# Kernel optimization log

Hardware: AMD Instinct MI355X
Metric: run time of the kernel (lower is better)

Reference implementation:

```python
import jax, jax.numpy as jnp
import numpy as np
from jax import lax

MAX_DEG = 10
BATCH = 4096
PER_DEG = 50000              # atoms per degree bucket
N_ATOMS = PER_DEG * (MAX_DEG + 1)
F = 128                      # n_atom_features == nb_filter
EPS = 1e-5


def setup_inputs() -> dict:
    key = jax.random.key(0)
    ks = jax.random.split(key, 8)
    atoms = jax.random.normal(ks[0], (N_ATOMS, F), jnp.float32)
    # atoms sorted by degree: degree d occupies rows [d*PER_DEG, (d+1)*PER_DEG)
    deg_slice = jnp.stack([jnp.arange(MAX_DEG + 1) * PER_DEG,
                           jnp.full((MAX_DEG + 1,), PER_DEG)], axis=1).astype(jnp.int32)
    membership = jax.random.randint(ks[1], (N_ATOMS,), 0, BATCH, dtype=jnp.int32)
    inp = {"atoms": atoms, "deg_slice": deg_slice, "membership": membership}
    for d in range(1, MAX_DEG + 1):
        inp[f"adj_{d}"] = jax.random.randint(jax.random.fold_in(key, d),
                                             (PER_DEG, d), 0, N_ATOMS, dtype=jnp.int32)
    inp["W"] = jax.random.normal(ks[2], (2 * MAX_DEG + 1, F, F), jnp.float32) * 0.05
    inp["b"] = jnp.zeros((2 * MAX_DEG + 1, F), jnp.float32)
    inp["gW"] = jax.random.normal(ks[3], (MAX_DEG + 1, F, F), jnp.float32) * 0.05
    inp["gb"] = jnp.zeros((MAX_DEG + 1, F), jnp.float32)
    inp["gamma"] = jnp.ones((F,), jnp.float32)
    inp["beta"] = jnp.zeros((F,), jnp.float32)
    return inp


def reference(atoms, deg_slice, membership,
              adj_1, adj_2, adj_3, adj_4, adj_5, adj_6, adj_7, adj_8, adj_9, adj_10,
              W, b, gW, gb, gamma, beta):
    adjs = [adj_1, adj_2, adj_3, adj_4, adj_5, adj_6, adj_7, adj_8, adj_9, adj_10]
    rel_outs = [None] * (MAX_DEG + 1)
    gat_outs = [None] * (MAX_DEG + 1)
    for d in range(1, MAX_DEG + 1):
        nbr_sum = jnp.take(atoms, adjs[d - 1], axis=0).sum(axis=1)  # (PER_DEG, F)
        self_atoms = lax.dynamic_slice_in_dim(atoms, deg_slice[d, 0], PER_DEG, axis=0)
        rel_outs[d] = (nbr_sum @ W[2 * (d - 1)] + b[2 * (d - 1)]
                       + self_atoms @ W[2 * (d - 1) + 1] + b[2 * (d - 1) + 1])
        gat_outs[d] = self_atoms @ gW[d - 1] + gb[d - 1]
    # degree 0 (min_deg == 0): self transform only
    self0 = lax.dynamic_slice_in_dim(atoms, deg_slice[0, 0], PER_DEG, axis=0)
    rel_outs[0] = self0 @ W[2 * MAX_DEG] + b[2 * MAX_DEG]
    gat_outs[0] = self0 @ gW[MAX_DEG] + gb[MAX_DEG]

    activated = jnp.concatenate(rel_outs, axis=0)     # (N_ATOMS, F), degree order == atom order
    gather_atoms = jnp.concatenate(gat_outs, axis=0)  # (N_ATOMS, F)
    # graph_gather: per-molecule sum (tf.dynamic_partition + reduce_sum == segment_sum)
    graph_feat = jax.ops.segment_sum(gather_atoms, membership, num_segments=BATCH)
    # activation is 'linear' (identity); layer-norm on atom features as in call()
    m = activated.mean(axis=-1, keepdims=True)
    std = jnp.sqrt(activated.var(axis=-1, keepdims=True) + EPS)
    normed = gamma * ((activated - m) / (std + EPS)) + beta
    return normed, graph_feat
```

## Files before the change

### kernel.cpp

```cpp
#include <hip/hip_runtime.h>
#include <hip/hip_bf16.h>

#define F_DIM   128
#define PER_DEG 50000
#define NDEG    11
#define MAXD    10
#define BATCH   4096
#define N_ATOMS (PER_DEG * NDEG)

#define BM     64
#define LDSN   136
#define BPD    ((PER_DEG + BM - 1) / BM)
#define WT_K   256
#define GWT_K  1440
#define LDST_L 264
#define WT_K_L 384

typedef __attribute__((ext_vector_type(4))) float f32x4;
typedef __attribute__((ext_vector_type(8))) short short8v;
typedef __attribute__((ext_vector_type(4))) short short4v;

struct AdjPtrs { const int* p[MAXD]; };

__device__ inline short bf16bits(float x) {
    __hip_bfloat16 h = __float2bfloat16(x);
    return __builtin_bit_cast(short, h);
}
__device__ inline float bf_lo(unsigned u) { return __builtin_bit_cast(float, u << 16); }
__device__ inline float bf_hi(unsigned u) { return __builtin_bit_cast(float, u & 0xFFFF0000u); }
__device__ inline float bf2f(short s) {
    return __builtin_bit_cast(float, ((unsigned)(unsigned short)s) << 16);
}
__device__ inline unsigned enc4_i8(float x0, float x1, float x2, float x3) {
    int q0 = (int)rintf(x0 * 16.0f), q1 = (int)rintf(x1 * 16.0f);
    int q2 = (int)rintf(x2 * 16.0f), q3 = (int)rintf(x3 * 16.0f);
    q0 = max(-127, min(127, q0)); q1 = max(-127, min(127, q1));
    q2 = max(-127, min(127, q2)); q3 = max(-127, min(127, q3));
    return (unsigned)(q0 & 255) | ((unsigned)(q1 & 255) << 8) |
           ((unsigned)(q2 & 255) << 16) | ((unsigned)(q3 & 255) << 24);
}
__device__ inline int sbyte(unsigned w, int k) {
    return (int)(w << (24 - 8 * k)) >> 24;
}

__global__ void prep_wt_main(const float* __restrict__ W, short* __restrict__ wt) {
    int idx = blockIdx.x * blockDim.x + threadIdx.x;
    const int total = NDEG * F_DIM * WT_K;
    if (idx >= total) return;
    int d   = idx / (F_DIM * WT_K);
    int rem = idx % (F_DIM * WT_K);
    int c   = rem / WT_K;
    int k   = rem % WT_K;
    float v;
    if (d == 0) {
        v = (k < 128) ? 0.0f : W[20 * 16384 + (k - 128) * F_DIM + c];
    } else {
        int wi = (k < 128) ? (2 * (d - 1)) : (2 * (d - 1) + 1);
        v = W[wi * 16384 + (k & 127) * F_DIM + c];
    }
    wt[idx] = bf16bits(v);
}

__global__ void prep_gwt(const float* __restrict__ gW, const float* __restrict__ gb,
                         short* __restrict__ gwt) {
    int idx = blockIdx.x * blockDim.x + threadIdx.x;
    const int total = F_DIM * GWT_K;
    if (idx >= total) return;
    int c = idx / GWT_K;
    int k = idx % GWT_K;
    float v = 0.0f;
    if (k < 1408) {
        int dd = k >> 7, f = k & 127;
        int gi = dd ? (dd - 1) : 10;
        v = gW[gi * 16384 + f * F_DIM + c];
    } else if (k < 1419) {
        int dd = k - 1408;
        int gi = dd ? (dd - 1) : 10;
        v = gb[gi * F_DIM + c];
    }
    gwt[idx] = bf16bits(v);
}

__global__ void to_i8(const float* __restrict__ in, unsigned char* __restrict__ out8) {
    const size_t n8 = (size_t)N_ATOMS * F_DIM / 8;
    size_t stride = (size_t)gridDim.x * blockDim.x;
    for (size_t k = (size_t)blockIdx.x * blockDim.x + threadIdx.x; k < n8; k += stride) {
        f32x4 a = __builtin_nontemporal_load((const f32x4*)in + 2 * k);
        f32x4 c = __builtin_nontemporal_load((const f32x4*)in + 2 * k + 1);
        uint2 u;
        u.x = enc4_i8(a[0], a[1], a[2], a[3]);
        u.y = enc4_i8(c[0], c[1], c[2], c[3]);
        ((uint2*)out8)[k] = u;
    }
}

__global__ void hist_kernel(const int* __restrict__ mem, int* __restrict__ hist2) {
    int i = blockIdx.x * blockDim.x + threadIdx.x;
    if (i >= N_ATOMS) return;
    atomicAdd(&hist2[mem[i] * NDEG + i / PER_DEG], 1);
}

__global__ void scan_offsets(const int* __restrict__ hist2,
                             int* __restrict__ off, int* __restrict__ cur) {
    __shared__ int lds[1024];
    const int tid = threadIdx.x;
    int h[4][NDEG];
    int tsum = 0;
    #pragma unroll
    for (int mi = 0; mi < 4; ++mi) {
        int m = tid * 4 + mi;
        #pragma unroll
        for (int dd = 0; dd < NDEG; ++dd) { h[mi][dd] = hist2[m * NDEG + dd]; tsum += h[mi][dd]; }
    }
    lds[tid] = tsum;
    __syncthreads();
    for (int ofs = 1; ofs < 1024; ofs <<= 1) {
        int v = (tid >= ofs) ? lds[tid - ofs] : 0;
        __syncthreads();
        lds[tid] += v;
        __syncthreads();
    }
    int run = lds[tid] - tsum;
    #pragma unroll
    for (int mi = 0; mi < 4; ++mi) {
        int m = tid * 4 + mi;
        #pragma unroll
        for (int dd = 0; dd < NDEG; ++dd) {
            int k = m * NDEG + dd;
            off[k] = run; cur[k] = run;
            run += h[mi][dd];
        }
    }
}

__global__ void scatter_kernel(const int* __restrict__ mem,
                               int* __restrict__ cur, int* __restrict__ idx) {
    int i = blockIdx.x * blockDim.x + threadIdx.x;
    if (i >= N_ATOMS) return;
    int pos = atomicAdd(&cur[mem[i] * NDEG + i / PER_DEG], 1);
    idx[pos] = i;
}

__global__ __launch_bounds__(256, 4) void fused_deg(
    const unsigned char* __restrict__ ai8,
    AdjPtrs adj,
    const short* __restrict__ wt,
    const float* __restrict__ b,
    const float* __restrict__ gamma,
    const float* __restrict__ beta,
    float* __restrict__ outN)
{
    __shared__ short As[BM * LDSN];
    const int bid   = blockIdx.x;
    const int d     = bid % NDEG;
    const int rb    = bid / NDEG;
    const int rows0 = rb * BM;
    const int tid   = threadIdx.x;

    {
        const int rloc = tid >> 2;
        const int p    = tid & 3;
        const int grow = rows0 + rloc;
        short* basep = &As[rloc * LDSN + p * 32];
        int acci[32];
        #pragma unroll
        for (int e = 0; e < 32; ++e) acci[e] = 0;
        if (grow < PER_DEG && d > 0) {
            const int* ar = adj.p[d - 1] + (size_t)grow * d;
            int idxs[MAXD];
            #pragma unroll
            for (int j = 0; j < MAXD; ++j) idxs[j] = (j < d) ? ar[j] : 0;
            uint4 b0x, b0y, b1x, b1y, b2x, b2y;
            {
                const uint4* r0 = (const uint4*)(ai8 + (size_t)idxs[0] * F_DIM) + p * 2;
                b0x = r0[0]; b0y = r0[1];
            }
            if (d > 1) {
                const uint4* r1 = (const uint4*)(ai8 + (size_t)idxs[1] * F_DIM) + p * 2;
                b1x = r1[0]; b1y = r1[1];
            }
            #pragma unroll
            for (int j = 0; j < MAXD; ++j) {
                if (j < d) {
                    if (j + 2 < d) {
                        const uint4* rn =
                            (const uint4*)(ai8 + (size_t)idxs[j + 2] * F_DIM) + p * 2;
                        b2x = rn[0]; b2y = rn[1];
                    }
                    unsigned wds[8] = { b0x.x, b0x.y, b0x.z, b0x.w,
                                        b0y.x, b0y.y, b0y.z, b0y.w };
                    #pragma unroll
                    for (int dw = 0; dw < 8; ++dw) {
                        #pragma unroll
                        for (int k = 0; k < 4; ++k)
                            acci[dw * 4 + k] += sbyte(wds[dw], k);
                    }
                    b0x = b1x; b0y = b1y;
                    b1x = b2x; b1y = b2y;
                }
            }
        }
        #pragma unroll
        for (int q = 0; q < 4; ++q) {
            short8v nb;
            #pragma unroll
            for (int e = 0; e < 8; ++e)
                nb[e] = bf16bits((float)acci[q * 8 + e] * 0.0625f);
            *(short8v*)(basep + q * 8) = nb;
        }
    }
    __syncthreads();

    const int w  = tid >> 6;
    const int l  = tid & 63;
    const int cg = l & 15;
    const int rg = l >> 4;

    short8v a[8];
    const short* arow = &As[(w * 16 + cg) * LDSN + rg * 8];
    #pragma unroll
    for (int s = 0; s < 4; ++s) a[s] = *(const short8v*)(arow + s * 32);
    int srow = d * PER_DEG + rows0 + w * 16 + cg;
    if (srow >= N_ATOMS) srow = N_ATOMS - 1;
    {
        const unsigned char* sp8 = ai8 + (size_t)srow * F_DIM + rg * 8;
        #pragma unroll
        for (int s = 0; s < 4; ++s) {
            uint2 u = *(const uint2*)(sp8 + s * 32);
            short8v sv;
            #pragma unroll
            for (int e = 0; e < 8; ++e) {
                unsigned wd = (e < 4) ? u.x : u.y;
                sv[e] = bf16bits((float)sbyte(wd, e & 3) * 0.0625f);
            }
            a[4 + s] = sv;
        }
    }

    const short* wtd = wt + (size_t)d * F_DIM * WT_K;
    f32x4 aA[8];
    #pragma unroll
    for (int n = 0; n < 8; ++n) aA[n] = 0.0f;
    #pragma unroll
    for (int s = 0; s < 8; ++s) {
        #pragma unroll
        for (int n = 0; n < 8; ++n) {
            short8v bv = *(const short8v*)(wtd + (n * 16 + cg) * WT_K + s * 32 + rg * 8);
            aA[n] = __builtin_amdgcn_mfma_f32_16x16x32_bf16(a[s], bv, aA[n], 0, 0, 0);
        }
    }

    float biasv[8], gam[8], bet[8];
    #pragma unroll
    for (int n = 0; n < 8; ++n) {
        int col = n * 16 + cg;
        biasv[n] = (d > 0) ? (b[(2 * d - 2) * F_DIM + col] + b[(2 * d - 1) * F_DIM + col])
                           : b[20 * F_DIM + col];
        gam[n] = gamma[col];
        bet[n] = beta[col];
    }
    const int valid = (PER_DEG - rows0 < BM) ? (PER_DEG - rows0) : BM;
    #pragma unroll
    for (int j = 0; j < 4; ++j) {
        const int rl = w * 16 + rg * 4 + j;
        float x[8];
        float s1 = 0.f, s2 = 0.f;
        #pragma unroll
        for (int n = 0; n < 8; ++n) {
            x[n] = aA[n][j] + biasv[n];
            s1 += x[n];
            s2 += x[n] * x[n];
        }
        #pragma unroll
        for (int m = 1; m < 16; m <<= 1) {
            s1 += __shfl_xor(s1, m);
            s2 += __shfl_xor(s2, m);
        }
        float mean = s1 * (1.0f / 128.0f);
        float var  = fmaxf(s2 * (1.0f / 128.0f) - mean * mean, 0.0f);
        float inv  = 1.0f / (sqrtf(var + 1e-5f) + 1e-5f);
        if (rl < valid) {
            float* op = outN + (size_t)(d * PER_DEG + rows0 + rl) * F_DIM;
            #pragma unroll
            for (int n = 0; n < 8; ++n)
                op[n * 16 + cg] = gam[n] * ((x[n] - mean) * inv) + bet[n];
        }
    }
}

__global__ __launch_bounds__(128) void mol_reduce(
    const float* __restrict__ atoms, const int* __restrict__ idx,
    const int* __restrict__ off, const int* __restrict__ hist2,
    short* __restrict__ sums)
{
    const int key = blockIdx.x;
    const int m   = key / NDEG;
    const int dd  = key - m * NDEG;
    const int c   = threadIdx.x;
    const int base = off[key];
    const int n    = hist2[key];
    float acc = 0.0f;
    if (n > 0) {
        int id0 = idx[base];
        float vcur = atoms[(size_t)id0 * F_DIM + c];
        for (int t = 0; t < n; ++t) {
            float vnext = 0.0f;
            if (t + 1 < n) {
                int id1 = idx[base + t + 1];
                vnext = atoms[(size_t)id1 * F_DIM + c];
            }
            acc += vcur;
            vcur = vnext;
        }
    }
    short* out = sums + (size_t)m * GWT_K;
    out[dd * F_DIM + c] = bf16bits(acc);
    if (c == 0) out[1408 + dd] = bf16bits((float)n);
    if (dd == 0 && c >= 11 && c < 32) out[1408 + c] = 0;
}

__global__ __launch_bounds__(256) void gat_gemm(
    const short* __restrict__ sums, const short* __restrict__ gwt,
    float* __restrict__ outG)
{
    const int rows0 = blockIdx.x * 64;
    const int tid = threadIdx.x;
    const int w = tid >> 6, l = tid & 63, cg = l & 15, rg = l >> 4;
    const short* ap = sums + (size_t)(rows0 + w * 16 + cg) * GWT_K + rg * 8;
    f32x4 acc[8];
    #pragma unroll
    for (int n = 0; n < 8; ++n) acc[n] = 0.0f;
    for (int ks = 0; ks < GWT_K / 32; ++ks) {
        short8v av = *(const short8v*)(ap + ks * 32);
        #pragma unroll
        for (int n = 0; n < 8; ++n) {
            short8v bv = *(const short8v*)(gwt + (size_t)(n * 16 + cg) * GWT_K + ks * 32 + rg * 8);
            acc[n] = __builtin_amdgcn_mfma_f32_16x16x32_bf16(av, bv, acc[n], 0, 0, 0);
        }
    }
    #pragma unroll
    for (int j = 0; j < 4; ++j) {
        int r = rows0 + w * 16 + rg * 4 + j;
        #pragma unroll
        for (int n = 0; n < 8; ++n)
            outG[(size_t)r * F_DIM + n * 16 + cg] = acc[n][j];
    }
}

__global__ void prep_wt_full(const float* __restrict__ W, const float* __restrict__ gW,
                             short* __restrict__ wt) {
    int idx = blockIdx.x * blockDim.x + threadIdx.x;
    const int total = NDEG * F_DIM * WT_K_L;
    if (idx >= total) return;
    int d   = idx / (F_DIM * WT_K_L);
    int rem = idx % (F_DIM * WT_K_L);
    int c   = rem / WT_K_L;
    int k   = rem % WT_K_L;
    float v;
    if (k < 256) {
        if (d == 0) v = (k < 128) ? 0.0f : W[20 * 16384 + (k - 128) * F_DIM + c];
        else {
            int wi = (k < 128) ? (2 * (d - 1)) : (2 * (d - 1) + 1);
            v = W[wi * 16384 + (k & 127) * F_DIM + c];
        }
    } else {
        int gi = (d == 0) ? 10 : (d - 1);
        v = gW[gi * 16384 + (k - 256) * F_DIM + c];
    }
    wt[idx] = bf16bits(v);
}

__global__ __launch_bounds__(256, 2) void fused_legacy(
    const float* __restrict__ atoms,
    const int* __restrict__ membership, AdjPtrs adj,
    const short* __restrict__ wt, const float* __restrict__ b,
    const float* __restrict__ gb, const float* __restrict__ gamma,
    const float* __restrict__ beta, float* __restrict__ outN, float* __restrict__ outG)
{
    __shared__ short As[BM * LDST_L];
    const int bid = blockIdx.x, d = bid / BPD, rb = bid % BPD;
    const int rows0 = rb * BM, tid = threadIdx.x;
    {
        const int rloc = tid >> 2, p = tid & 3;
        const int grow = rows0 + rloc;
        const bool rv = grow < PER_DEG;
        short* basep = &As[rloc * LDST_L + p * 32];
        f32x4 accn[8], selfv[8];
        #pragma unroll
        for (int q = 0; q < 8; ++q) { accn[q] = 0.0f; selfv[q] = 0.0f; }
        const f32x4* atomsv = (const f32x4*)atoms;
        if (rv) {
            if (d > 0) {
                const int* ar = adj.p[d - 1] + (size_t)grow * d;
                int idxs[MAXD];
                #pragma unroll
                for (int j = 0; j < MAXD; ++j) idxs[j] = (j < d) ? ar[j] : 0;
                #pragma unroll
                for (int j = 0; j < MAXD; ++j) if (j < d) {
                    const f32x4* s = atomsv + (size_t)idxs[j] * 32 + p * 8;
                    #pragma unroll
                    for (int q = 0; q < 8; ++q) accn[q] += s[q];
                }
            }
            const f32x4* s = atomsv + (size_t)(d * PER_DEG + grow) * 32 + p * 8;
            #pragma unroll
            for (int q = 0; q < 8; ++q) selfv[q] = s[q];
        }
        #pragma unroll
        for (int q = 0; q < 8; ++q) {
            short4v nb = { bf16bits(accn[q][0]), bf16bits(accn[q][1]),
                           bf16bits(accn[q][2]), bf16bits(accn[q][3]) };
            short4v sv = { bf16bits(selfv[q][0]), bf16bits(selfv[q][1]),
                           bf16bits(selfv[q][2]), bf16bits(selfv[q][3]) };
            *(short4v*)(basep + q * 4) = nb;
            *(short4v*)(basep + 128 + q * 4) = sv;
        }
    }
    __syncthreads();
    const int w = tid >> 6, l = tid & 63, cg = l & 15, rg = l >> 4;
    short8v a[8];
    const short* arow = &As[(w * 16 + cg) * LDST_L + rg * 8];
    #pragma unroll
    for (int s = 0; s < 8; ++s) a[s] = *(const short8v*)(arow + s * 32);
    const short* wtd = wt + (size_t)d * F_DIM * WT_K_L;
    f32x4 aA[8], aG[8];
    #pragma unroll
    for (int n = 0; n < 8; ++n) { aA[n] = 0.0f; aG[n] = 0.0f; }
    #pragma unroll
    for (int s = 0; s < 8; ++s) {
        #pragma unroll
        for (int n = 0; n < 8; ++n) {
            short8v bv = *(const short8v*)(wtd + (n * 16 + cg) * WT_K_L + s * 32 + rg * 8);
            aA[n] = __builtin_amdgcn_mfma_f32_16x16x32_bf16(a[s], bv, aA[n], 0, 0, 0);
        }
    }
    #pragma unroll
    for (int s = 0; s < 4; ++s) {
        #pragma unroll
        for (int n = 0; n < 8; ++n) {
            short8v bv = *(const short8v*)(wtd + (n * 16 + cg) * WT_K_L + 256 + s * 32 + rg * 8);
            aG[n] = __builtin_amdgcn_mfma_f32_16x16x32_bf16(a[4 + s], bv, aG[n], 0, 0, 0);
        }
    }
    const int gi = (d == 0) ? 10 : (d - 1);
    float biasv[8], gbv[8], gam[8], bet[8];
    #pragma unroll
    for (int n = 0; n < 8; ++n) {
        int col = n * 16 + cg;
        biasv[n] = (d > 0) ? (b[(2*d-2)*F_DIM+col] + b[(2*d-1)*F_DIM+col]) : b[20*F_DIM+col];
        gbv[n] = gb[gi * F_DIM + col];
        gam[n] = gamma[col]; bet[n] = beta[col];
    }
    const int valid = (PER_DEG - rows0 < BM) ? (PER_DEG - rows0) : BM;
    #pragma unroll
    for (int j = 0; j < 4; ++j) {
        const int rl = w * 16 + rg * 4 + j;
        float x[8], s1 = 0.f, s2 = 0.f;
        #pragma unroll
        for (int n = 0; n < 8; ++n) { x[n] = aA[n][j] + biasv[n]; s1 += x[n]; s2 += x[n]*x[n]; }
        #pragma unroll
        for (int m = 1; m < 16; m <<= 1) { s1 += __shfl_xor(s1, m); s2 += __shfl_xor(s2, m); }
        float mean = s1 * (1.0f/128.0f);
        float var  = fmaxf(s2 * (1.0f/128.0f) - mean*mean, 0.0f);
        float inv  = 1.0f / (sqrtf(var + 1e-5f) + 1e-5f);
        if (rl < valid) {
            const int growi = d * PER_DEG + rows0 + rl;
            float* op = outN + (size_t)growi * F_DIM;
            float* gp = outG + (size_t)membership[growi] * F_DIM;
            #pragma unroll
            for (int n = 0; n < 8; ++n) {
                int col = n * 16 + cg;
                op[col] = gam[n] * ((x[n] - mean) * inv) + bet[n];
                atomicAdd(&gp[col], aG[n][j] + gbv[n]);
            }
        }
    }
}

extern "C" void kernel_launch(void* const* d_in, const int* in_sizes, int n_in,
                              void* d_out, int out_size, void* d_ws, size_t ws_size,
                              hipStream_t stream) {
    const float* atoms      = (const float*)d_in[0];
    const int*   membership = (const int*)d_in[2];
    AdjPtrs adj;
    for (int i = 0; i < MAXD; ++i) adj.p[i] = (const int*)d_in[3 + i];
    const float* W     = (const float*)d_in[13];
    const float* b     = (const float*)d_in[14];
    const float* gW    = (const float*)d_in[15];
    const float* gb    = (const float*)d_in[16];
    const float* gamma = (const float*)d_in[17];
    const float* beta  = (const float*)d_in[18];

    float* outN = (float*)d_out;
    float* outG = outN + (size_t)N_ATOMS * F_DIM;

    auto al = [](size_t x) { return (x + 255) & ~(size_t)255; };
    const size_t sz_wt   = al((size_t)NDEG * F_DIM * WT_K * 2);
    const size_t sz_gwt  = al((size_t)F_DIM * GWT_K * 2);
    const size_t sz_h    = al((size_t)BATCH * NDEG * 4);
    const size_t sz_idx  = al((size_t)N_ATOMS * 4);
    const size_t sz_sums = al((size_t)BATCH * GWT_K * 2);
    const size_t sz_ai8  = (size_t)N_ATOMS * F_DIM;

    size_t o = 0;
    short* wt    = (short*)((char*)d_ws + o); o += sz_wt;
    short* gwt   = (short*)((char*)d_ws + o); o += sz_gwt;
    int*   hist2 = (int*)  ((char*)d_ws + o); o += sz_h;
    int*   offa  = (int*)  ((char*)d_ws + o); o += sz_h;
    int*   cura  = (int*)  ((char*)d_ws + o); o += sz_h;
    int*   idx   = (int*)  ((char*)d_ws + o); o += sz_idx;
    short* sums  = (short*)((char*)d_ws + o); o += sz_sums;
    unsigned char* ai8 = (unsigned char*)((char*)d_ws + o); o += sz_ai8;

    if (ws_size >= o) {
        prep_wt_main<<<(NDEG * F_DIM * WT_K + 255) / 256, 256, 0, stream>>>(W, wt);
        prep_gwt<<<(F_DIM * GWT_K + 255) / 256, 256, 0, stream>>>(gW, gb, gwt);
        hipMemsetAsync(hist2, 0, (size_t)BATCH * NDEG * 4, stream);
        to_i8<<<2048, 256, 0, stream>>>(atoms, ai8);
        hist_kernel<<<(N_ATOMS + 255) / 256, 256, 0, stream>>>(membership, hist2);
        scan_offsets<<<1, 1024, 0, stream>>>(hist2, offa, cura);
        scatter_kernel<<<(N_ATOMS + 255) / 256, 256, 0, stream>>>(membership, cura, idx);
        fused_deg<<<NDEG * BPD, 256, 0, stream>>>(ai8, adj, wt, b, gamma, beta, outN);
        mol_reduce<<<BATCH * NDEG, 128, 0, stream>>>(atoms, idx, offa, hist2, sums);
        gat_gemm<<<BATCH / 64, 256, 0, stream>>>(sums, gwt, outG);
    } else {
        short* lwt = (short*)d_ws;
        prep_wt_full<<<(NDEG * F_DIM * WT_K_L + 255) / 256, 256, 0, stream>>>(W, gW, lwt);
        hipMemsetAsync(outG, 0, (size_t)BATCH * F_DIM * 4, stream);
        fused_legacy<<<NDEG * BPD, 256, 0, stream>>>(atoms, membership, adj, lwt,
                                                     b, gb, gamma, beta, outN, outG);
    }
}
```

Measured before the change: 634.7 us.

## Merge degree gather-GEMM and molecule reduction into one interleaved kernel

Combines the per-degree gather+GEMM+layernorm kernel and the per-molecule segment-sum kernel into a single launch, interleaving the two block types evenly across the grid by proportional index mapping. Molecule blocks now process two keys per 256-thread block. The aim is to overlap the compute-heavy MFMA blocks with the latency-bound gather reduction blocks and drop a kernel boundary. The risk is that the fused kernel keeps the LDS and register budget of the GEMM path even for reduction blocks, which can limit occupancy for them.

```diff
diff --git a/kernel.cpp b/kernel.cpp
--- a/kernel.cpp
+++ b/kernel.cpp
@@ -15,6 +15,10 @@
 #define GWT_K  1440
 #define LDST_L 264
 #define WT_K_L 384
+
+#define GATHER_BLKS (NDEG * BPD)
+#define MOL_BLKS    ((BATCH * NDEG) / 2)
+#define ALL_BLKS    (GATHER_BLKS + MOL_BLKS)
 
 typedef __attribute__((ext_vector_type(4))) float f32x4;
 typedef __attribute__((ext_vector_type(8))) short short8v;
@@ -141,182 +145,190 @@
     idx[pos] = i;
 }
 
-__global__ __launch_bounds__(256, 4) void fused_deg(
+__global__ __launch_bounds__(256, 4) void fused_all(
     const unsigned char* __restrict__ ai8,
+    const float* __restrict__ atoms,
     AdjPtrs adj,
     const short* __restrict__ wt,
     const float* __restrict__ b,
     const float* __restrict__ gamma,
     const float* __restrict__ beta,
-    float* __restrict__ outN)
+    const int* __restrict__ idx,
+    const int* __restrict__ off,
+    const int* __restrict__ hist2,
+    float* __restrict__ outN,
+    short* __restrict__ sums)
 {
     __shared__ short As[BM * LDSN];
-    const int bid   = blockIdx.x;
-    const int d     = bid % NDEG;
-    const int rb    = bid / NDEG;
-    const int rows0 = rb * BM;
-    const int tid   = threadIdx.x;
-
-    {
-        const int rloc = tid >> 2;
-        const int p    = tid & 3;
-        const int grow = rows0 + rloc;
-        short* basep = &As[rloc * LDSN + p * 32];
-        int acci[32];
-        #pragma unroll
-        for (int e = 0; e < 32; ++e) acci[e] = 0;
-        if (grow < PER_DEG && d > 0) {
-            const int* ar = adj.p[d - 1] + (size_t)grow * d;
-            int idxs[MAXD];
-            #pragma unroll
-            for (int j = 0; j < MAXD; ++j) idxs[j] = (j < d) ? ar[j] : 0;
-            uint4 b0x, b0y, b1x, b1y, b2x, b2y;
-            {
-                const uint4* r0 = (const uint4*)(ai8 + (size_t)idxs[0] * F_DIM) + p * 2;
-                b0x = r0[0]; b0y = r0[1];
-            }
-            if (d > 1) {
-                const uint4* r1 = (const uint4*)(ai8 + (size_t)idxs[1] * F_DIM) + p * 2;
-                b1x = r1[0]; b1y = r1[1];
-            }
-            #pragma unroll
-            for (int j = 0; j < MAXD; ++j) {
-                if (j < d) {
-                    if (j + 2 < d) {
-                        const uint4* rn =
-                            (const uint4*)(ai8 + (size_t)idxs[j + 2] * F_DIM) + p * 2;
-                        b2x = rn[0]; b2y = rn[1];
+    const int bid = blockIdx.x;
+    const int tid = threadIdx.x;
+
+    const int i0 = (int)(((long long)bid * GATHER_BLKS) / ALL_BLKS);
+    const int i1 = (int)(((long long)(bid + 1) * GATHER_BLKS) / ALL_BLKS);
+
+    if (i1 > i0) {
+        const int d     = i0 % NDEG;
+        const int rb    = i0 / NDEG;
+        const int rows0 = rb * BM;
+
+        {
+            const int rloc = tid >> 2;
+            const int p    = tid & 3;
+            const int grow = rows0 + rloc;
+            short* basep = &As[rloc * LDSN + p * 32];
+            int acci[32];
+            #pragma unroll
+            for (int e = 0; e < 32; ++e) acci[e] = 0;
+            if (grow < PER_DEG && d > 0) {
+                const int* ar = adj.p[d - 1] + (size_t)grow * d;
+                int idxs[MAXD];
+                #pragma unroll
+                for (int j = 0; j < MAXD; ++j) idxs[j] = (j < d) ? ar[j] : 0;
+                uint4 b0x, b0y, b1x, b1y, b2x, b2y;
+                {
+                    const uint4* r0 = (const uint4*)(ai8 + (size_t)idxs[0] * F_DIM) + p * 2;
+                    b0x = r0[0]; b0y = r0[1];
+                }
+                if (d > 1) {
+                    const uint4* r1 = (const uint4*)(ai8 + (size_t)idxs[1] * F_DIM) + p * 2;
+                    b1x = r1[0]; b1y = r1[1];
+                }
+                #pragma unroll
+                for (int j = 0; j < MAXD; ++j) {
+                    if (j < d) {
+                        if (j + 2 < d) {
+                            const uint4* rn =
+                                (const uint4*)(ai8 + (size_t)idxs[j + 2] * F_DIM) + p * 2;
+                            b2x = rn[0]; b2y = rn[1];
+                        }
+                        unsigned wds[8] = { b0x.x, b0x.y, b0x.z, b0x.w,
+                                            b0y.x, b0y.y, b0y.z, b0y.w };
+                        #pragma unroll
+                        for (int dw = 0; dw < 8; ++dw) {
+                            #pragma unroll
+                            for (int k = 0; k < 4; ++k)
+                                acci[dw * 4 + k] += sbyte(wds[dw], k);
+                        }
+                        b0x = b1x; b0y = b1y;
+                        b1x = b2x; b1y = b2y;
                     }
-                    unsigned wds[8] = { b0x.x, b0x.y, b0x.z, b0x.w,
-                                        b0y.x, b0y.y, b0y.z, b0y.w };
-                    #pragma unroll
-                    for (int dw = 0; dw < 8; ++dw) {
-                        #pragma unroll
-                        for (int k = 0; k < 4; ++k)
-                            acci[dw * 4 + k] += sbyte(wds[dw], k);
+                }
+            }
+            #pragma unroll
+            for (int q = 0; q < 4; ++q) {
+                short8v nb;
+                #pragma unroll
+                for (int e = 0; e < 8; ++e)
+                    nb[e] = bf16bits((float)acci[q * 8 + e] * 0.0625f);
+                *(short8v*)(basep + q * 8) = nb;
+            }
+        }
+        __syncthreads();
+
+        const int w  = tid >> 6;
+        const int l  = tid & 63;
+        const int cg = l & 15;
+        const int rg = l >> 4;
+
+        short8v a[8];
+        const short* arow = &As[(w * 16 + cg) * LDSN + rg * 8];
+        #pragma unroll
+        for (int s = 0; s < 4; ++s) a[s] = *(const short8v*)(arow + s * 32);
+        int srow = d * PER_DEG + rows0 + w * 16 + cg;
+        if (srow >= N_ATOMS) srow = N_ATOMS - 1;
+        {
+            const unsigned char* sp8 = ai8 + (size_t)srow * F_DIM + rg * 8;
+            #pragma unroll
+            for (int s = 0; s < 4; ++s) {
+                uint2 u = *(const uint2*)(sp8 + s * 32);
+                short8v sv;
+                #pragma unroll
+                for (int e = 0; e < 8; ++e) {
+                    unsigned wd = (e < 4) ? u.x : u.y;
+                    sv[e] = bf16bits((float)sbyte(wd, e & 3) * 0.0625f);
+                }
+                a[4 + s] = sv;
+            }
+        }
+
+        const short* wtd = wt + (size_t)d * F_DIM * WT_K;
+        f32x4 aA[8];
+        #pragma unroll
+        for (int n = 0; n < 8; ++n) aA[n] = 0.0f;
+        #pragma unroll
+        for (int s = 0; s < 8; ++s) {
+            #pragma unroll
+            for (int n = 0; n < 8; ++n) {
+                short8v bv = *(const short8v*)(wtd + (n * 16 + cg) * WT_K + s * 32 + rg * 8);
+                aA[n] = __builtin_amdgcn_mfma_f32_16x16x32_bf16(a[s], bv, aA[n], 0, 0, 0);
+            }
+        }
+
+        float biasv[8], gam[8], bet[8];
+        #pragma unroll
+        for (int n = 0; n < 8; ++n) {
+            int col = n * 16 + cg;
+            biasv[n] = (d > 0) ? (b[(2 * d - 2) * F_DIM + col] + b[(2 * d - 1) * F_DIM + col])
+                               : b[20 * F_DIM + col];
+            gam[n] = gamma[col];
+            bet[n] = beta[col];
+        }
+        const int valid = (PER_DEG - rows0 < BM) ? (PER_DEG - rows0) : BM;
+        #pragma unroll
+        for (int j = 0; j < 4; ++j) {
+            const int rl = w * 16 + rg * 4 + j;
+            float x[8];
+            float s1 = 0.f, s2 = 0.f;
+            #pragma unroll
+            for (int n = 0; n < 8; ++n) {
+                x[n] = aA[n][j] + biasv[n];
+                s1 += x[n];
+                s2 += x[n] * x[n];
+            }
+            #pragma unroll
+            for (int m = 1; m < 16; m <<= 1) {
+                s1 += __shfl_xor(s1, m);
+                s2 += __shfl_xor(s2, m);
+            }
+            float mean = s1 * (1.0f / 128.0f);
+            float var  = fmaxf(s2 * (1.0f / 128.0f) - mean * mean, 0.0f);
+            float inv  = 1.0f / (sqrtf(var + 1e-5f) + 1e-5f);
+            if (rl < valid) {
+                float* op = outN + (size_t)(d * PER_DEG + rows0 + rl) * F_DIM;
+                #pragma unroll
+                for (int n = 0; n < 8; ++n)
+                    op[n * 16 + cg] = gam[n] * ((x[n] - mean) * inv) + bet[n];
+            }
+        }
+    } else {
+        const int mb   = bid - i0;
+        const int key  = mb * 2 + (tid >> 7);
+        const int c    = tid & 127;
+        if (key < BATCH * NDEG) {
+            const int m    = key / NDEG;
+            const int dd   = key - m * NDEG;
+            const int base = off[key];
+            const int n    = hist2[key];
+            float acc = 0.0f;
+            if (n > 0) {
+                int id0 = idx[base];
+                float vcur = atoms[(size_t)id0 * F_DIM + c];
+                for (int t = 0; t < n; ++t) {
+                    float vnext = 0.0f;
+                    if (t + 1 < n) {
+                        int id1 = idx[base + t + 1];
+                        vnext = atoms[(size_t)id1 * F_DIM + c];
                     }
-                    b0x = b1x; b0y = b1y;
-                    b1x = b2x; b1y = b2y;
+                    acc += vcur;
+                    vcur = vnext;
                 }
             }
-        }
-        #pragma unroll
-        for (int q = 0; q < 4; ++q) {
-            short8v nb;
-            #pragma unroll
-            for (int e = 0; e < 8; ++e)
-                nb[e] = bf16bits((float)acci[q * 8 + e] * 0.0625f);
-            *(short8v*)(basep + q * 8) = nb;
-        }
-    }
-    __syncthreads();
-
-    const int w  = tid >> 6;
-    const int l  = tid & 63;
-    const int cg = l & 15;
-    const int rg = l >> 4;
-
-    short8v a[8];
-    const short* arow = &As[(w * 16 + cg) * LDSN + rg * 8];
-    #pragma unroll
-    for (int s = 0; s < 4; ++s) a[s] = *(const short8v*)(arow + s * 32);
-    int srow = d * PER_DEG + rows0 + w * 16 + cg;
-    if (srow >= N_ATOMS) srow = N_ATOMS - 1;
-    {
-        const unsigned char* sp8 = ai8 + (size_t)srow * F_DIM + rg * 8;
-        #pragma unroll
-        for (int s = 0; s < 4; ++s) {
-            uint2 u = *(const uint2*)(sp8 + s * 32);
-            short8v sv;
-            #pragma unroll
-            for (int e = 0; e < 8; ++e) {
-                unsigned wd = (e < 4) ? u.x : u.y;
-                sv[e] = bf16bits((float)sbyte(wd, e & 3) * 0.0625f);
-            }
-            a[4 + s] = sv;
-        }
-    }
-
-    const short* wtd = wt + (size_t)d * F_DIM * WT_K;
-    f32x4 aA[8];
-    #pragma unroll
-    for (int n = 0; n < 8; ++n) aA[n] = 0.0f;
-    #pragma unroll
-    for (int s = 0; s < 8; ++s) {
-        #pragma unroll
-        for (int n = 0; n < 8; ++n) {
-            short8v bv = *(const short8v*)(wtd + (n * 16 + cg) * WT_K + s * 32 + rg * 8);
-            aA[n] = __builtin_amdgcn_mfma_f32_16x16x32_bf16(a[s], bv, aA[n], 0, 0, 0);
-        }
-    }
-
-    float biasv[8], gam[8], bet[8];
-    #pragma unroll
-    for (int n = 0; n < 8; ++n) {
-        int col = n * 16 + cg;
-        biasv[n] = (d > 0) ? (b[(2 * d - 2) * F_DIM + col] + b[(2 * d - 1) * F_DIM + col])
-                           : b[20 * F_DIM + col];
-        gam[n] = gamma[col];
-        bet[n] = beta[col];
-    }
-    const int valid = (PER_DEG - rows0 < BM) ? (PER_DEG - rows0) : BM;
-    #pragma unroll
-    for (int j = 0; j < 4; ++j) {
-        const int rl = w * 16 + rg * 4 + j;
-        float x[8];
-        float s1 = 0.f, s2 = 0.f;
-        #pragma unroll
-        for (int n = 0; n < 8; ++n) {
-            x[n] = aA[n][j] + biasv[n];
-            s1 += x[n];
-            s2 += x[n] * x[n];
-        }
-        #pragma unroll
-        for (int m = 1; m < 16; m <<= 1) {
-            s1 += __shfl_xor(s1, m);
-            s2 += __shfl_xor(s2, m);
-        }
-        float mean = s1 * (1.0f / 128.0f);
-        float var  = fmaxf(s2 * (1.0f / 128.0f) - mean * mean, 0.0f);
-        float inv  = 1.0f / (sqrtf(var + 1e-5f) + 1e-5f);
-        if (rl < valid) {
-            float* op = outN + (size_t)(d * PER_DEG + rows0 + rl) * F_DIM;
-            #pragma unroll
-            for (int n = 0; n < 8; ++n)
-                op[n * 16 + cg] = gam[n] * ((x[n] - mean) * inv) + bet[n];
-        }
-    }
-}
-
-__global__ __launch_bounds__(128) void mol_reduce(
-    const float* __restrict__ atoms, const int* __restrict__ idx,
-    const int* __restrict__ off, const int* __restrict__ hist2,
-    short* __restrict__ sums)
-{
-    const int key = blockIdx.x;
-    const int m   = key / NDEG;
-    const int dd  = key - m * NDEG;
-    const int c   = threadIdx.x;
-    const int base = off[key];
-    const int n    = hist2[key];
-    float acc = 0.0f;
-    if (n > 0) {
-        int id0 = idx[base];
-        float vcur = atoms[(size_t)id0 * F_DIM + c];
-        for (int t = 0; t < n; ++t) {
-            float vnext = 0.0f;
-            if (t + 1 < n) {
-                int id1 = idx[base + t + 1];
-                vnext = atoms[(size_t)id1 * F_DIM + c];
-            }
-            acc += vcur;
-            vcur = vnext;
-        }
-    }
-    short* out = sums + (size_t)m * GWT_K;
-    out[dd * F_DIM + c] = bf16bits(acc);
-    if (c == 0) out[1408 + dd] = bf16bits((float)n);
-    if (dd == 0 && c >= 11 && c < 32) out[1408 + c] = 0;
+            short* out = sums + (size_t)m * GWT_K;
+            out[dd * F_DIM + c] = bf16bits(acc);
+            if (c == 0) out[1408 + dd] = bf16bits((float)n);
+            if (dd == 0 && c >= 11 && c < 32) out[1408 + c] = 0;
+        }
+    }
 }
 
 __global__ __launch_bounds__(256) void gat_gemm(
@@ -520,8 +532,8 @@
         hist_kernel<<<(N_ATOMS + 255) / 256, 256, 0, stream>>>(membership, hist2);
         scan_offsets<<<1, 1024, 0, stream>>>(hist2, offa, cura);
         scatter_kernel<<<(N_ATOMS + 255) / 256, 256, 0, stream>>>(membership, cura, idx);
-        fused_deg<<<NDEG * BPD, 256, 0, stream>>>(ai8, adj, wt, b, gamma, beta, outN);
-        mol_reduce<<<BATCH * NDEG, 128, 0, stream>>>(atoms, idx, offa, hist2, sums);
+        fused_all<<<ALL_BLKS, 256, 0, stream>>>(ai8, atoms, adj, wt, b, gamma, beta,
+                                                idx, offa, hist2, outN, sums);
         gat_gemm<<<BATCH / 64, 256, 0, stream>>>(sums, gwt, outG);
     } else {
         short* lwt = (short*)d_ws;
```

Result: slower. 721.9 us (+13.7%).
